# Performance work log

Hardware: AMD Instinct MI355X
Metric: run time of the kernel (lower is better)

Reference implementation:

```python
import jax, jax.numpy as jnp
import numpy as np

D_IN, D_K, D_V = 1024, 1024, 1024
B, S = 4, 2048

def setup_inputs() -> dict:
    key = jax.random.key(0)
    ks = jax.random.split(key, 7)
    s = 1.0 / np.sqrt(D_IN)
    return {
        "x": jax.random.normal(ks[0], (B, S, D_IN), dtype=jnp.float32),
        "Wq": jax.random.uniform(ks[1], (D_IN, D_K), jnp.float32, -s, s),
        "bq": jax.random.uniform(ks[2], (D_K,), jnp.float32, -s, s),
        "Wk": jax.random.uniform(ks[3], (D_IN, D_K), jnp.float32, -s, s),
        "bk": jax.random.uniform(ks[4], (D_K,), jnp.float32, -s, s),
        "Wv": jax.random.uniform(ks[5], (D_IN, D_V), jnp.float32, -s, s),
        "bv": jax.random.uniform(ks[6], (D_V,), jnp.float32, -s, s),
    }

def reference(x, Wq, bq, Wk, bk, Wv, bv):
    # QKV projections: [B,S,d_in] @ [d_in,d] + b
    Q = x @ Wq + bq  # [B,S,d_k]
    K = x @ Wk + bk  # [B,S,d_k]
    V = x @ Wv + bv  # [B,S,d_v]
    # Non-standard recipe: softmax over UNSCALED scores, then divide output by sqrt(d_k)
    scores = jnp.einsum('bqd,bkd->bqk', Q, K)  # [B,S,S]
    attn = jax.nn.softmax(scores, axis=2)
    out = jnp.einsum('bqk,bkv->bqv', attn, V) / jnp.sqrt(jnp.asarray(K.shape[2], dtype=x.dtype))
    return out
```

## Files before the change

kernel.cpp:

```cpp
#include <hip/hip_runtime.h>
#include <stdint.h>

typedef unsigned short u16;
typedef _Float16 f16;
typedef _Float16 f16x8 __attribute__((ext_vector_type(8)));
typedef float f32x4 __attribute__((ext_vector_type(4)));

#define DIN 1024
#define SEQ 2048
#define NB 4
#define MB (1u << 20)


__device__ __forceinline__ void gload_lds16(const void* g, void* l) {
    __builtin_amdgcn_global_load_lds(
        (__attribute__((address_space(1))) void*)(uintptr_t)g,
        (__attribute__((address_space(3))) void*)l,
        16, 0, 0);
}

__device__ __forceinline__ int xcd_swz(int h, int cpx) {
    return (h & 7) * cpx + (h >> 3);
}

__device__ __forceinline__ void barrier_raw() {
    asm volatile("" ::: "memory");
    __builtin_amdgcn_s_barrier();
    asm volatile("" ::: "memory");
}
template<int N>
__device__ __forceinline__ void wait_lgkm() {
    asm volatile("s_waitcnt lgkmcnt(%0)" :: "i"(N) : "memory");
    __builtin_amdgcn_sched_barrier(0);
}
template<int N>
__device__ __forceinline__ void wait_vm() {
    asm volatile("s_waitcnt vmcnt(%0)" :: "i"(N) : "memory");
}


__device__ __forceinline__ void gemm256(
    const char* __restrict__ A, const char* __restrict__ B,
    int ldab, int ldbb, int nt, char* smem, f32x4 acc[8][4])
{
    const int tid  = threadIdx.x;
    const int lane = tid & 63;
    const int wave = tid >> 6;
    const int ln15 = lane & 15;
    const int k16  = (lane >> 4) << 4;
    const int wmB  = (wave >> 2) * 128;
    const int wnB  = (wave & 3) * 64;

    #pragma unroll
    for (int m = 0; m < 8; ++m)
        #pragma unroll
        for (int n = 0; n < 4; ++n)
            acc[m][n] = (f32x4){0.f, 0.f, 0.f, 0.f};

    const char* pA[2];
    const char* pB[2];
    #pragma unroll
    for (int i = 0; i < 2; ++i) {
        const int La = i * 8192 + tid * 16;
        const int r  = La >> 7;
        const int sc = (La & 127) ^ ((r & 7) << 4);
        pA[i] = A + (size_t)r * ldab + sc;
        pB[i] = B + (size_t)r * ldbb + sc;
    }
    const int ldsw = wave * 1024;

    f16x8 a0[4][2], a1[4][2], b[4][2];

    auto stage = [&](int g) {
        if (g < 4 * nt) {
            const int ks  = g >> 2;
            const int isB = ((g & 2) == 0);
            const int h   = g & 1;
            char* l = smem + (ks & 1) * 65536 + (isB ? 32768 : 0) + h * 16384 + ldsw;
            #pragma unroll
            for (int i = 0; i < 2; ++i) {
                const char* gp = (isB ? pB[i] + (size_t)(h * 128) * ldbb
                                      : pA[i] + (size_t)(h * 128) * ldab) + ks * 128;
                gload_lds16(gp, l + i * 8192);
            }
        }
    };

#define RDA0(base) { _Pragma("unroll") for (int mf = 0; mf < 4; ++mf) { \
        const int r = wmB + mf * 16 + ln15; \
        const int sw = (r & 7) << 4; \
        const char* p = (base) + r * 128; \
        a0[mf][0] = *(const f16x8*)(p + (k16 ^ sw)); \
        a0[mf][1] = *(const f16x8*)(p + ((64 + k16) ^ sw)); } }

#define RDA1(base) { _Pragma("unroll") for (int mf = 0; mf < 4; ++mf) { \
        const int r = wmB + (mf + 4) * 16 + ln15; \
        const int sw = (r & 7) << 4; \
        const char* p = (base) + r * 128; \
        a1[mf][0] = *(const f16x8*)(p + (k16 ^ sw)); \
        a1[mf][1] = *(const f16x8*)(p + ((64 + k16) ^ sw)); } }

#define RDB2(nf0, base) { _Pragma("unroll") for (int nf = (nf0); nf < (nf0) + 2; ++nf) { \
        const int r = wnB + nf * 16 + ln15; \
        const int sw = (r & 7) << 4; \
        const char* p = (base) + r * 128; \
        b[nf][0] = *(const f16x8*)(p + (k16 ^ sw)); \
        b[nf][1] = *(const f16x8*)(p + ((64 + k16) ^ sw)); } }

#define MM(aa, aoff, nf0) { __builtin_amdgcn_s_setprio(1); \
        _Pragma("unroll") for (int mf = 0; mf < 4; ++mf) \
        _Pragma("unroll") for (int nf = (nf0); nf < (nf0) + 2; ++nf) { \
            acc[(aoff) + mf][nf] = __builtin_amdgcn_mfma_f32_16x16x32_f16( \
                aa[mf][0], b[nf][0], acc[(aoff) + mf][nf], 0, 0, 0); \
            acc[(aoff) + mf][nf] = __builtin_amdgcn_mfma_f32_16x16x32_f16( \
                aa[mf][1], b[nf][1], acc[(aoff) + mf][nf], 0, 0, 0); } \
        __builtin_amdgcn_s_setprio(0); }

    #pragma unroll
    for (int g = 0; g < 8; ++g) stage(g);
    wait_vm<8>();
    barrier_raw();
    RDA0(smem);

    for (int t = 0; t < nt; ++t) {
        const char* sAc = smem + (t & 1) * 65536;
        const char* sBc = sAc + 32768;
        const char* sAn = smem + ((t + 1) & 1) * 65536;
        const int gb = 4 * (t + 2);

        RDB2(0, sBc);
        __builtin_amdgcn_sched_barrier(0);
        RDB2(2, sBc);
        barrier_raw(); wait_lgkm<4>(); MM(a0, 0, 0); barrier_raw();

        RDA1(sAc);
        barrier_raw(); wait_lgkm<8>(); MM(a0, 0, 2); barrier_raw();

        stage(gb + 0); stage(gb + 1);
        if (t < nt - 2) { wait_vm<4>(); } else if (t == nt - 2) { wait_vm<0>(); }
        barrier_raw(); wait_lgkm<0>(); MM(a1, 4, 0); barrier_raw();

        RDA0(sAn);
        stage(gb + 2); stage(gb + 3);
        barrier_raw(); MM(a1, 4, 2); barrier_raw();
    }
#undef RDA0
#undef RDA1
#undef RDB2
#undef MM
}


__device__ __forceinline__ void gemm_tile(
    const char* __restrict__ A, const char* __restrict__ B,
    int lda, int ldb, int ksteps, char* smem, f32x4 acc[4][4])
{
    const int lane = threadIdx.x & 63;
    const int wave = threadIdx.x >> 6;

    #pragma unroll
    for (int m = 0; m < 4; ++m)
        #pragma unroll
        for (int n = 0; n < 4; ++n)
            acc[m][n] = (f32x4){0.f, 0.f, 0.f, 0.f};

    const char* ga[4];
    const char* gb[4];
    int ldsoff[4];
    #pragma unroll
    for (int i = 0; i < 4; ++i) {
        int La = (wave * 4 + i) * 1024 + lane * 16;
        int r  = La >> 7;
        int cb = La & 127;
        int sc = cb ^ ((r & 7) << 4);
        ga[i] = A + (size_t)r * (size_t)(lda * 2) + sc;
        gb[i] = B + (size_t)r * (size_t)(ldb * 2) + sc;
        ldsoff[i] = (wave * 4 + i) * 1024;
    }

    const int wr = (wave >> 1) * 64;
    const int wc = (wave & 1) * 64;

    for (int ks = 0; ks < ksteps; ++ks) {
        #pragma unroll
        for (int i = 0; i < 4; ++i) {
            gload_lds16(ga[i], smem + ldsoff[i]);
            gload_lds16(gb[i], smem + 16384 + ldsoff[i]);
            ga[i] += 128;
            gb[i] += 128;
        }
        __syncthreads();

        #pragma unroll
        for (int kk = 0; kk < 2; ++kk) {
            const int kb = kk * 64 + ((lane >> 4) << 4);
            f16x8 af[4], bfv[4];
            #pragma unroll
            for (int m = 0; m < 4; ++m) {
                int r = wr + m * 16 + (lane & 15);
                af[m] = *(const f16x8*)(smem + r * 128 + (kb ^ ((r & 7) << 4)));
            }
            #pragma unroll
            for (int n = 0; n < 4; ++n) {
                int r = wc + n * 16 + (lane & 15);
                bfv[n] = *(const f16x8*)(smem + 16384 + r * 128 + (kb ^ ((r & 7) << 4)));
            }
            #pragma unroll
            for (int m = 0; m < 4; ++m)
                #pragma unroll
                for (int n = 0; n < 4; ++n)
                    acc[m][n] = __builtin_amdgcn_mfma_f32_16x16x32_f16(
                        af[m], bfv[n], acc[m][n], 0, 0, 0);
        }
        __syncthreads();
    }
}


__global__ __launch_bounds__(256) void k_prep(
    const float* __restrict__ x, f16* __restrict__ xh,
    const float* __restrict__ Wq, const float* __restrict__ Wk,
    const float* __restrict__ Wv, f16* __restrict__ wt)
{
    __shared__ float tile[32][33];
    const int bid = blockIdx.x;
    if (bid < 2048) {
        const int n8 = (NB * SEQ * DIN) / 8;
        for (int idx = bid * 256 + threadIdx.x; idx < n8; idx += 2048 * 256) {
            f32x4 a = ((const f32x4*)x)[(size_t)idx * 2];
            f32x4 b = ((const f32x4*)x)[(size_t)idx * 2 + 1];
            f16x8 o;
            o[0] = (f16)a[0]; o[1] = (f16)a[1]; o[2] = (f16)a[2]; o[3] = (f16)a[3];
            o[4] = (f16)b[0]; o[5] = (f16)b[1]; o[6] = (f16)b[2]; o[7] = (f16)b[3];
            ((f16x8*)xh)[idx] = o;
        }
    } else {
        const int wb = bid - 2048;
        const int mtx = wb >> 10;
        const int rem = wb & 1023;
        const int n0 = (rem & 31) * 32, k0 = (rem >> 5) * 32;
        const float* W = (mtx == 0) ? Wq : (mtx == 1 ? Wk : Wv);
        const int c = threadIdx.x & 31, r0 = threadIdx.x >> 5;
        #pragma unroll
        for (int rr = r0; rr < 32; rr += 8)
            tile[rr][c] = W[(size_t)(k0 + rr) * DIN + n0 + c];
        __syncthreads();
        f16* o = wt + (size_t)mtx * DIN * DIN;
        #pragma unroll
        for (int rr = r0; rr < 32; rr += 8)
            o[(size_t)(n0 + rr) * DIN + k0 + c] = (f16)tile[c][rr];
    }
}

__global__ __launch_bounds__(512, 2) void k_gemm_qkv8(
    const f16* __restrict__ xh, const f16* __restrict__ wt,
    const float* __restrict__ bq, const float* __restrict__ bk,
    const float* __restrict__ bv,
    f16* __restrict__ Q, f16* __restrict__ K, f16* __restrict__ Vt)
{
    extern __shared__ char smem[];
    f32x4 acc[8][4];
    const int sid = xcd_swz(blockIdx.x, 48);
    const int blkN = sid % 12;
    const int blkM = sid / 12;
    gemm256((const char*)(xh + (size_t)blkM * 256 * DIN),
            (const char*)(wt + (size_t)blkN * 256 * DIN),
            DIN * 2, DIN * 2, DIN / 64, smem, acc);

    const int lane = threadIdx.x & 63;
    const int wave = threadIdx.x >> 6;
    const int row0 = blkM * 256 + (wave >> 2) * 128;
    const int col0 = blkN * 256 + (wave & 3) * 64;

    if (col0 >= 2048) {
        const int bb = row0 >> 11;
        const int sb = row0 & (SEQ - 1);
        f16* Vtb = Vt + (size_t)bb * DIN * SEQ;
        #pragma unroll
        for (int n = 0; n < 4; ++n) {
            int d = (col0 - 2048) + n * 16 + (lane & 15);
            float bias = bv[d];
            #pragma unroll
            for (int m = 0; m < 8; ++m) {
                #pragma unroll
                for (int j = 0; j < 4; ++j) {
                    int s = sb + m * 16 + (lane >> 4) * 4 + j;
                    Vtb[(size_t)d * SEQ + s] = (f16)(acc[m][n][j] + bias);
                }
            }
        }
    } else {
        f16* dst = (col0 < 1024) ? Q : K;
        const float* bsrc = (col0 < 1024) ? bq : bk;
        const int ncb = col0 & 1023;
        #pragma unroll
        for (int n = 0; n < 4; ++n) {
            int nc = ncb + n * 16 + (lane & 15);
            float bias = bsrc[nc];
            #pragma unroll
            for (int m = 0; m < 8; ++m) {
                #pragma unroll
                for (int j = 0; j < 4; ++j) {
                    int row = row0 + m * 16 + (lane >> 4) * 4 + j;
                    dst[(size_t)row * 1024 + nc] = (f16)(acc[m][n][j] + bias);
                }
            }
        }
    }
}

__global__ __launch_bounds__(512, 2) void k_gemm_scores8(
    const f16* __restrict__ Q, const f16* __restrict__ K, float* __restrict__ S)
{
    extern __shared__ char smem[];
    f32x4 acc[8][4];
    const int sid = xcd_swz(blockIdx.x, 32);
    const int bx = sid & 7, by = (sid >> 3) & 7, b = sid >> 6;
    const f16* Qb = Q + (size_t)b * SEQ * DIN;
    const f16* Kb = K + (size_t)b * SEQ * DIN;
    gemm256((const char*)(Qb + (size_t)by * 256 * DIN),
            (const char*)(Kb + (size_t)bx * 256 * DIN),
            DIN * 2, DIN * 2, DIN / 64, smem, acc);

    float* Sb = S + (size_t)b * SEQ * SEQ;
    const int lane = threadIdx.x & 63;
    const int wave = threadIdx.x >> 6;
    const int row0 = by * 256 + (wave >> 2) * 128;
    const int col0 = bx * 256 + (wave & 3) * 64;
    #pragma unroll
    for (int m = 0; m < 8; ++m)
        #pragma unroll
        for (int n = 0; n < 4; ++n) {
            int col = col0 + n * 16 + (lane & 15);
            #pragma unroll
            for (int j = 0; j < 4; ++j) {
                int row = row0 + m * 16 + (lane >> 4) * 4 + j;
                Sb[(size_t)row * SEQ + col] = acc[m][n][j];
            }
        }
}

__global__ __launch_bounds__(256) void k_softmax(
    const float* __restrict__ S, f16* __restrict__ P)
{
    const size_t row = blockIdx.x;
    const float* s = S + row * SEQ;
    f16* p = P + row * SEQ;
    const int t = threadIdx.x;

    f32x4 x0 = ((const f32x4*)s)[t * 2];
    f32x4 x1 = ((const f32x4*)s)[t * 2 + 1];
    float v[8] = {x0[0], x0[1], x0[2], x0[3], x1[0], x1[1], x1[2], x1[3]};

    float mx = v[0];
    #pragma unroll
    for (int j = 1; j < 8; ++j) mx = fmaxf(mx, v[j]);
    #pragma unroll
    for (int o = 32; o; o >>= 1) mx = fmaxf(mx, __shfl_xor(mx, o, 64));
    __shared__ float red[8];
    if ((t & 63) == 0) red[t >> 6] = mx;
    __syncthreads();
    mx = fmaxf(fmaxf(red[0], red[1]), fmaxf(red[2], red[3]));

    float sum = 0.f;
    #pragma unroll
    for (int j = 0; j < 8; ++j) { v[j] = __expf(v[j] - mx); sum += v[j]; }
    #pragma unroll
    for (int o = 32; o; o >>= 1) sum += __shfl_xor(sum, o, 64);
    if ((t & 63) == 0) red[4 + (t >> 6)] = sum;
    __syncthreads();
    sum = (red[4] + red[5]) + (red[6] + red[7]);
    float inv = 1.0f / sum;

    f16x8 o8;
    #pragma unroll
    for (int j = 0; j < 8; ++j) o8[j] = (f16)(v[j] * inv);
    ((f16x8*)p)[t] = o8;
}

__global__ __launch_bounds__(256) void k_gemm_pv(
    const f16* __restrict__ P, const f16* __restrict__ Vt, float* __restrict__ out)
{
    __shared__ __align__(16) char smem[32768];
    f32x4 acc[4][4];
    const int sid = xcd_swz(blockIdx.x, 64);
    const int bx = sid & 7;
    const int by = (sid >> 3) & 15;
    const int b  = sid >> 7;
    const f16* Pb  = P  + (size_t)b * SEQ * SEQ;
    const f16* Vtb = Vt + (size_t)b * 1024 * SEQ;
    gemm_tile((const char*)(Pb  + (size_t)by * 128 * SEQ),
              (const char*)(Vtb + (size_t)bx * 128 * SEQ),
              SEQ, SEQ, SEQ / 64, smem, acc);

    float* ob = out + (size_t)b * SEQ * 1024;
    const int lane = threadIdx.x & 63;
    const int wave = threadIdx.x >> 6;
    const int row0 = by * 128 + (wave >> 1) * 64;
    const int col0 = bx * 128 + (wave & 1) * 64;
    #pragma unroll
    for (int m = 0; m < 4; ++m)
        #pragma unroll
        for (int n = 0; n < 4; ++n) {
            int col = col0 + n * 16 + (lane & 15);
            #pragma unroll
            for (int j = 0; j < 4; ++j) {
                int row = row0 + m * 16 + (lane >> 4) * 4 + j;
                ob[(size_t)row * 1024 + col] = acc[m][n][j] * 0.03125f;
            }
        }
}


extern "C" void kernel_launch(void* const* d_in, const int* in_sizes, int n_in,
                              void* d_out, int out_size, void* d_ws, size_t ws_size,
                              hipStream_t stream) {
    const float* x  = (const float*)d_in[0];
    const float* Wq = (const float*)d_in[1];
    const float* bq = (const float*)d_in[2];
    const float* Wk = (const float*)d_in[3];
    const float* bk = (const float*)d_in[4];
    const float* Wv = (const float*)d_in[5];
    const float* bv = (const float*)d_in[6];
    float* out = (float*)d_out;
    char* ws = (char*)d_ws;

    f16*  Q  = (f16*)(ws);
    f16*  K  = (f16*)(ws + (size_t)16 * MB);
    f16*  Vt = (f16*)(ws + (size_t)32 * MB);
    f16*  xh = (f16*)(ws + (size_t)48 * MB);
    f16*  wt = (f16*)(ws + (size_t)64 * MB);
    float* S = (float*)(ws + (size_t)48 * MB);
    f16*  P  = Q;

    const size_t needed = (size_t)112 * MB;
    if (ws_size < needed) return;

    hipFuncSetAttribute((const void*)k_gemm_qkv8,
                        hipFuncAttributeMaxDynamicSharedMemorySize, 131072);
    hipFuncSetAttribute((const void*)k_gemm_scores8,
                        hipFuncAttributeMaxDynamicSharedMemorySize, 131072);

    k_prep<<<5120, 256, 0, stream>>>(x, xh, Wq, Wk, Wv, wt);
    k_gemm_qkv8<<<384, 512, 131072, stream>>>(xh, wt, bq, bk, bv, Q, K, Vt);
    k_gemm_scores8<<<256, 512, 131072, stream>>>(Q, K, S);
    k_softmax<<<NB * SEQ, 256, 0, stream>>>(S, P);
    k_gemm_pv<<<512, 256, 0, stream>>>(P, Vt, out);
}
```

Baseline: 176.1 us.

## Store attention scores in fp16 and fold output scale into softmax

The scores GEMM now writes S as fp16 instead of fp32, and softmax reads fp16. This halves the bytes of the large BxSxS intermediate that is written and then read back. The 1/sqrt(d_k) scale moves from the PV epilogue into the softmax normalisation. Separately, the QKV projection GEMM switches from 256x256 tiles with 512 threads and dynamic LDS to 128x128 tiles with 256 threads and more blocks. The main risk is precision: unscaled scores stored in fp16 lose absolute accuracy, and that error passes through exp.

```diff
diff --git a/kernel.cpp b/kernel.cpp
--- a/kernel.cpp
+++ b/kernel.cpp
@@ -252,25 +252,25 @@
     }
 }
 
-__global__ __launch_bounds__(512, 2) void k_gemm_qkv8(
+__global__ __launch_bounds__(256) void k_gemm_qkv(
     const f16* __restrict__ xh, const f16* __restrict__ wt,
     const float* __restrict__ bq, const float* __restrict__ bk,
     const float* __restrict__ bv,
     f16* __restrict__ Q, f16* __restrict__ K, f16* __restrict__ Vt)
 {
-    extern __shared__ char smem[];
-    f32x4 acc[8][4];
-    const int sid = xcd_swz(blockIdx.x, 48);
-    const int blkN = sid % 12;
-    const int blkM = sid / 12;
-    gemm256((const char*)(xh + (size_t)blkM * 256 * DIN),
-            (const char*)(wt + (size_t)blkN * 256 * DIN),
-            DIN * 2, DIN * 2, DIN / 64, smem, acc);
+    __shared__ __align__(16) char smem[32768];
+    f32x4 acc[4][4];
+    const int sid = xcd_swz(blockIdx.x, 192);
+    const int blkN = sid % 24;
+    const int blkM = sid / 24;
+    gemm_tile((const char*)(xh + (size_t)blkM * 128 * DIN),
+              (const char*)(wt + (size_t)blkN * 128 * DIN),
+              DIN, DIN, DIN / 64, smem, acc);
 
     const int lane = threadIdx.x & 63;
     const int wave = threadIdx.x >> 6;
-    const int row0 = blkM * 256 + (wave >> 2) * 128;
-    const int col0 = blkN * 256 + (wave & 3) * 64;
+    const int row0 = blkM * 128 + (wave >> 1) * 64;
+    const int col0 = blkN * 128 + (wave & 1) * 64;
 
     if (col0 >= 2048) {
         const int bb = row0 >> 11;
@@ -281,7 +281,7 @@
             int d = (col0 - 2048) + n * 16 + (lane & 15);
             float bias = bv[d];
             #pragma unroll
-            for (int m = 0; m < 8; ++m) {
+            for (int m = 0; m < 4; ++m) {
                 #pragma unroll
                 for (int j = 0; j < 4; ++j) {
                     int s = sb + m * 16 + (lane >> 4) * 4 + j;
@@ -298,7 +298,7 @@
             int nc = ncb + n * 16 + (lane & 15);
             float bias = bsrc[nc];
             #pragma unroll
-            for (int m = 0; m < 8; ++m) {
+            for (int m = 0; m < 4; ++m) {
                 #pragma unroll
                 for (int j = 0; j < 4; ++j) {
                     int row = row0 + m * 16 + (lane >> 4) * 4 + j;
@@ -310,7 +310,7 @@
 }
 
 __global__ __launch_bounds__(512, 2) void k_gemm_scores8(
-    const f16* __restrict__ Q, const f16* __restrict__ K, float* __restrict__ S)
+    const f16* __restrict__ Q, const f16* __restrict__ K, f16* __restrict__ S)
 {
     extern __shared__ char smem[];
     f32x4 acc[8][4];
@@ -322,7 +322,7 @@
             (const char*)(Kb + (size_t)bx * 256 * DIN),
             DIN * 2, DIN * 2, DIN / 64, smem, acc);
 
-    float* Sb = S + (size_t)b * SEQ * SEQ;
+    f16* Sb = S + (size_t)b * SEQ * SEQ;
     const int lane = threadIdx.x & 63;
     const int wave = threadIdx.x >> 6;
     const int row0 = by * 256 + (wave >> 2) * 128;
@@ -335,22 +335,23 @@
             #pragma unroll
             for (int j = 0; j < 4; ++j) {
                 int row = row0 + m * 16 + (lane >> 4) * 4 + j;
-                Sb[(size_t)row * SEQ + col] = acc[m][n][j];
+                Sb[(size_t)row * SEQ + col] = (f16)acc[m][n][j];
             }
         }
 }
 
 __global__ __launch_bounds__(256) void k_softmax(
-    const float* __restrict__ S, f16* __restrict__ P)
+    const f16* __restrict__ S, f16* __restrict__ P)
 {
     const size_t row = blockIdx.x;
-    const float* s = S + row * SEQ;
+    const f16* s = S + row * SEQ;
     f16* p = P + row * SEQ;
     const int t = threadIdx.x;
 
-    f32x4 x0 = ((const f32x4*)s)[t * 2];
-    f32x4 x1 = ((const f32x4*)s)[t * 2 + 1];
-    float v[8] = {x0[0], x0[1], x0[2], x0[3], x1[0], x1[1], x1[2], x1[3]};
+    f16x8 xi = ((const f16x8*)s)[t];
+    float v[8];
+    #pragma unroll
+    for (int j = 0; j < 8; ++j) v[j] = (float)xi[j];
 
     float mx = v[0];
     #pragma unroll
@@ -370,11 +371,11 @@
     if ((t & 63) == 0) red[4 + (t >> 6)] = sum;
     __syncthreads();
     sum = (red[4] + red[5]) + (red[6] + red[7]);
-    float inv = 1.0f / sum;
+    float inv32 = 0.03125f / sum;
 
     f16x8 o8;
     #pragma unroll
-    for (int j = 0; j < 8; ++j) o8[j] = (f16)(v[j] * inv);
+    for (int j = 0; j < 8; ++j) o8[j] = (f16)(v[j] * inv32);
     ((f16x8*)p)[t] = o8;
 }
 
@@ -406,7 +407,7 @@
             #pragma unroll
             for (int j = 0; j < 4; ++j) {
                 int row = row0 + m * 16 + (lane >> 4) * 4 + j;
-                ob[(size_t)row * 1024 + col] = acc[m][n][j] * 0.03125f;
+                ob[(size_t)row * 1024 + col] = acc[m][n][j];
             }
         }
 }
@@ -430,19 +431,17 @@
     f16*  Vt = (f16*)(ws + (size_t)32 * MB);
     f16*  xh = (f16*)(ws + (size_t)48 * MB);
     f16*  wt = (f16*)(ws + (size_t)64 * MB);
-    float* S = (float*)(ws + (size_t)48 * MB);
+    f16*  S  = (f16*)(ws + (size_t)48 * MB);
     f16*  P  = Q;
 
-    const size_t needed = (size_t)112 * MB;
+    const size_t needed = (size_t)80 * MB;
     if (ws_size < needed) return;
 
-    hipFuncSetAttribute((const void*)k_gemm_qkv8,
-                        hipFuncAttributeMaxDynamicSharedMemorySize, 131072);
     hipFuncSetAttribute((const void*)k_gemm_scores8,
                         hipFuncAttributeMaxDynamicSharedMemorySize, 131072);
 
     k_prep<<<5120, 256, 0, stream>>>(x, xh, Wq, Wk, Wv, wt);
-    k_gemm_qkv8<<<384, 512, 131072, stream>>>(xh, wt, bq, bk, bv, Q, K, Vt);
+    k_gemm_qkv<<<1536, 256, 0, stream>>>(xh, wt, bq, bk, bv, Q, K, Vt);
     k_gemm_scores8<<<256, 512, 131072, stream>>>(Q, K, S);
     k_softmax<<<NB * SEQ, 256, 0, stream>>>(S, P);
     k_gemm_pv<<<512, 256, 0, stream>>>(P, Vt, out);
```

Measured after the change: 165.9 us. 5.8% less time.
